# Kernel optimization log

Measured on AMD Instinct MI355X. Metric: run time of the kernel, lower is better.

Reference implementation:

```python
import jax, jax.numpy as jnp
import numpy as np

N_NODES = 349525  # complete 4-ary tree, depth 10: (4**10 - 1) / 3
X_SIZE = 128
H_SIZE = 128


def setup_inputs() -> dict:
    key = jax.random.key(0)
    ks = jax.random.split(key, 6)
    s = 0.05  # keep gates out of saturation
    return {
        "x": jax.random.normal(ks[0], (N_NODES, X_SIZE), jnp.float32),
        "W_iou": jax.random.normal(ks[1], (X_SIZE, 3 * H_SIZE), jnp.float32) * s,
        "U_iou": jax.random.normal(ks[2], (H_SIZE, 3 * H_SIZE), jnp.float32) * s,
        "b_iou": jnp.zeros((3 * H_SIZE,), jnp.float32),
        "W_f": jax.random.normal(ks[3], (X_SIZE, H_SIZE), jnp.float32) * s,
        "U_f": jax.random.normal(ks[4], (H_SIZE, H_SIZE), jnp.float32) * s,
        "b_f": jnp.zeros((H_SIZE,), jnp.float32),
        "depth": 10,
        "branching": 4,
    }


def _apply_node(iou, c_sum):
    # apply_node_func: i,o,u gates then cell/hidden update
    i, o, u = jnp.split(iou, 3, axis=-1)
    c = jax.nn.sigmoid(i) * jnp.tanh(u) + c_sum
    h = jax.nn.sigmoid(o) * jnp.tanh(c)
    return h, c


def reference(x, W_iou, U_iou, b_iou, W_f, U_f, b_f, depth, branching):
    # Nodes are in BFS order of a complete `branching`-ary forest-tree;
    # level l occupies [off[l], off[l+1]) and the children of level l are
    # exactly level l+1 (contiguous, `branching` per parent).
    H = b_f.shape[-1]
    off = [(branching ** l - 1) // (branching - 1) for l in range(depth + 1)]

    node_iou = x @ W_iou + b_iou  # [N, 3H]  (W_iou(x) + b_iou)
    node_f = x @ W_f + b_f        # [N, H]   (W_f(x) + b_f)

    h_levels = [None] * depth
    c_levels = [None] * depth

    # Leaves: mailbox empty -> h_tilda = 0, c = 0
    s, e = off[depth - 1], off[depth]
    h, c = _apply_node(node_iou[s:e], jnp.zeros((e - s, H), x.dtype))
    h_levels[depth - 1], c_levels[depth - 1] = h, c

    # Bottom-up topological propagation
    for l in range(depth - 2, -1, -1):
        s, e = off[l], off[l + 1]
        nl = e - s
        ch_h = h_levels[l + 1].reshape(nl, branching, H)  # mailbox['h']
        ch_c = c_levels[l + 1].reshape(nl, branching, H)  # mailbox['c']
        h_tilda = ch_h.sum(axis=1)
        # f = sigmoid(U_f(mailbox.h) + node_f[:, None])
        f = jax.nn.sigmoid(jnp.einsum("nkh,hg->nkg", ch_h, U_f) + node_f[s:e][:, None, :])
        c_sum = (f * ch_c).sum(axis=1)
        iou = node_iou[s:e] + h_tilda @ U_iou
        h, c = _apply_node(iou, c_sum)
        h_levels[l], c_levels[l] = h, c

    h_all = jnp.concatenate(h_levels, axis=0)
    c_all = jnp.concatenate(c_levels, axis=0)
    return h_all, c_all
```

## Files before the change

kernel.cpp:

```cpp
#include <hip/hip_runtime.h>

#define H 128

typedef __bf16 bf16x8 __attribute__((ext_vector_type(8)));
typedef float f32x4 __attribute__((ext_vector_type(4)));

__device__ __forceinline__ float fsig(float x) {
  return __builtin_amdgcn_rcpf(1.0f + __expf(-x));
}
__device__ __forceinline__ float ftanh(float x) {
  float ax = fabsf(x), e = __expf(-2.0f * ax);
  float t = (1.0f - e) * __builtin_amdgcn_rcpf(1.0f + e);
  return x < 0.0f ? -t : t;
}
__device__ __forceinline__ uint2 pack4(float a, float b, float c, float d) {
  union { __bf16 h[4]; uint2 u; } r;
  r.h[0] = (__bf16)a; r.h[1] = (__bf16)b; r.h[2] = (__bf16)c; r.h[3] = (__bf16)d;
  return r.u;
}
__device__ __forceinline__ unsigned swz(unsigned row, unsigned colByte, unsigned rowBytes) {
  return (row * rowBytes + colByte) ^ ((row & 7) << 4);
}
__device__ __forceinline__ void gload_lds16(const void* g, void* lds) {
  __builtin_amdgcn_global_load_lds((const __attribute__((address_space(1))) void*)g,
                                   (__attribute__((address_space(3))) void*)lds, 16, 0, 0);
}

__global__ __launch_bounds__(256)
void prep_weights(const float* __restrict__ W_iou, const float* __restrict__ U_iou,
                  const float* __restrict__ W_f, const float* __restrict__ U_f,
                  uint4* __restrict__ ws)
{
  int item = blockIdx.x * 256 + threadIdx.x;
  float v[8];
  if (item < 2048) {
    int fj = item >> 8, rem = item & 255, ks = rem >> 6, lane = rem & 63;
    int n = fj * 16 + (lane & 15), kb = ks * 32 + (lane >> 4) * 8;
    #pragma unroll
    for (int j = 0; j < 8; j++) v[j] = U_f[(kb + j) * H + n];
  } else if (item < 4096) {
    int i2 = item - 2048;
    int fj = i2 >> 8, rem = i2 & 255, ks = rem >> 6, lane = rem & 63;
    int n = fj * 16 + (lane & 15), kb = ks * 32 + (lane >> 4) * 8;
    #pragma unroll
    for (int j = 0; j < 8; j++) v[j] = W_f[(kb + j) * H + n];
  } else {
    int i2 = item - 4096;
    int fj = i2 >> 9, rem = i2 & 511, ks = rem >> 6, lane = rem & 63;
    int col = (fj >> 3) * 128 + (fj & 7) * 16 + (lane & 15);
    int kb = ks * 32 + (lane >> 4) * 8;
    #pragma unroll
    for (int j = 0; j < 8; j++) {
      int k = kb + j;
      v[j] = (k < 128) ? W_iou[k * 384 + col] : U_iou[(k - 128) * 384 + col];
    }
  }
  union { __bf16 h[8]; uint4 u; } r;
  #pragma unroll
  for (int j = 0; j < 8; j++) r.h[j] = (__bf16)v[j];
  ws[item] = r.u;
}

__device__ __forceinline__ bf16x8 read_a_f32(const char* As, int row, int colB) {
  unsigned x1 = (unsigned)row * 512 + ((unsigned)colB ^ ((row & 7) << 4));
  unsigned x2 = (unsigned)row * 512 + ((unsigned)(colB + 16) ^ ((row & 7) << 4));
  f32x4 va = *reinterpret_cast<const f32x4*>(As + x1);
  f32x4 vb = *reinterpret_cast<const f32x4*>(As + x2);
  union { __bf16 h[8]; bf16x8 v; } u;
  u.h[0] = (__bf16)va.x; u.h[1] = (__bf16)va.y; u.h[2] = (__bf16)va.z; u.h[3] = (__bf16)va.w;
  u.h[4] = (__bf16)vb.x; u.h[5] = (__bf16)vb.y; u.h[6] = (__bf16)vb.z; u.h[7] = (__bf16)vb.w;
  return u.v;
}

template<bool WS>
__global__ __launch_bounds__(256)
void leaf6(const float* __restrict__ x, const __bf16* __restrict__ iou_fmt,
           const float* __restrict__ b_iou,
           float* __restrict__ h_glob, float* __restrict__ c_glob,
           __bf16* __restrict__ hbf, __bf16* __restrict__ htws, int leaf_start)
{
  __shared__ __align__(16) char As[64 * 512];
  const int t = threadIdx.x;
  const int bid = blockIdx.x;
  const int m0 = leaf_start + bid * 64;
  const int lane = t & 63, w = t >> 6;
  const int l15 = lane & 15, l4 = lane >> 4;

  {
    const char* xb = (const char*)(x + (size_t)m0 * H);
    #pragma unroll
    for (int i = 0; i < 8; i++) {
      int d = w * 8192 + i * 1024 + lane * 16;
      int row = d >> 9, c = d & 511;
      gload_lds16(xb + row * 512 + (c ^ ((row & 7) << 4)), As + w * 8192 + i * 1024);
    }
  }
  __syncthreads();

  #pragma unroll 1
  for (int j = 0; j < 2; j++) {
    f32x4 acc[4][3] = {};
    #pragma unroll
    for (int ks = 0; ks < 4; ks++) {
      bf16x8 a[4], b[3];
      #pragma unroll
      for (int m = 0; m < 4; m++)
        a[m] = read_a_f32(As, m * 16 + l15, ks * 128 + l4 * 32);
      #pragma unroll
      for (int g = 0; g < 3; g++) {
        int nf = g * 8 + 2 * w + j;
        b[g] = *reinterpret_cast<const bf16x8*>(iou_fmt + ((size_t)(nf * 8 + ks) * 64 + lane) * 8);
      }
      #pragma unroll
      for (int m = 0; m < 4; m++)
        #pragma unroll
        for (int g = 0; g < 3; g++)
          acc[m][g] = __builtin_amdgcn_mfma_f32_16x16x32_bf16(a[m], b[g], acc[m][g], 0, 0, 0);
    }

    int ch = (2 * w + j) * 16 + l15;
    float bi = b_iou[ch], bo = b_iou[H + ch], bu = b_iou[2 * H + ch];
    #pragma unroll
    for (int m = 0; m < 4; m++) {
      int rowb = m * 16 + l4 * 4;
      float hsum = 0.0f;
      #pragma unroll
      for (int r = 0; r < 4; r++) {
        size_t o = (size_t)(m0 + rowb + r) * H + ch;
        float c = fsig(acc[m][0][r] + bi) * ftanh(acc[m][2][r] + bu);
        float h = fsig(acc[m][1][r] + bo) * ftanh(c);
        h_glob[o] = h;
        c_glob[o] = c;
        if (WS) {
          int CR = bid * 64 + rowb + r;
          unsigned off = ((unsigned)(CR >> 7)) * 32768u + swz(CR & 127, ch * 2, 256);
          *reinterpret_cast<__bf16*>(reinterpret_cast<char*>(hbf) + off) = (__bf16)h;
          hsum += h;
        }
      }
      if (WS) htws[(size_t)(bid * 16 + m * 4 + l4) * H + ch] = (__bf16)hsum;
    }
  }
}

__device__ __forceinline__ void fused_core(
    const __bf16* __restrict__ uf_fmt, const __bf16* __restrict__ wf_fmt,
    const __bf16* __restrict__ iou_fmt,
    const float* __restrict__ b_iou, const float* __restrict__ b_f,
    float* __restrict__ h_glob, float* __restrict__ c_glob,
    int prow0, int crow0, int npar,
    char* CH, char* XH, float* SC)
{
  const int t = threadIdx.x;
  const int lane = t & 63, w = t >> 6;
  const int l15 = lane & 15, l4 = lane >> 4;

  {
    f32x4 acc[2][2] = {};
    #pragma unroll
    for (int ks = 0; ks < 4; ks++) {
      bf16x8 a[2], b[2];
      #pragma unroll
      for (int m = 0; m < 2; m++)
        a[m] = *reinterpret_cast<const bf16x8*>(XH + swz(m * 16 + l15, (ks * 32 + l4 * 8) * 2, 512));
      #pragma unroll
      for (int n = 0; n < 2; n++) {
        int nf = 2 * w + n;
        b[n] = *reinterpret_cast<const bf16x8*>(wf_fmt + ((size_t)(nf * 4 + ks) * 64 + lane) * 8);
      }
      #pragma unroll
      for (int m = 0; m < 2; m++)
        #pragma unroll
        for (int n = 0; n < 2; n++)
          acc[m][n] = __builtin_amdgcn_mfma_f32_16x16x32_bf16(a[m], b[n], acc[m][n], 0, 0, 0);
    }
    #pragma unroll
    for (int m = 0; m < 2; m++)
      #pragma unroll
      for (int n = 0; n < 2; n++)
        #pragma unroll
        for (int r = 0; r < 4; r++)
          SC[(m * 16 + l4 * 4 + r) * 128 + (2 * w + n) * 16 + l15] = acc[m][n][r];
  }
  __syncthreads();

  {
    f32x4 acc[2][8] = {};
    #pragma unroll
    for (int ks = 0; ks < 4; ks++) {
      bf16x8 a[2], b[8];
      #pragma unroll
      for (int m = 0; m < 2; m++)
        a[m] = *reinterpret_cast<const bf16x8*>(CH + swz(w * 32 + m * 16 + l15, (ks * 32 + l4 * 8) * 2, 256));
      #pragma unroll
      for (int n = 0; n < 8; n++)
        b[n] = *reinterpret_cast<const bf16x8*>(uf_fmt + ((size_t)(n * 4 + ks) * 64 + lane) * 8);
      #pragma unroll
      for (int m = 0; m < 2; m++)
        #pragma unroll
        for (int n = 0; n < 8; n++)
          acc[m][n] = __builtin_amdgcn_mfma_f32_16x16x32_bf16(a[m], b[n], acc[m][n], 0, 0, 0);
    }
    #pragma unroll
    for (int m = 0; m < 2; m++) {
      int rbase = w * 32 + m * 16 + l4 * 4;
      int ploc = rbase >> 2;
      #pragma unroll
      for (int n = 0; n < 8; n++) {
        int ch = n * 16 + l15;
        float sfx = SC[ploc * 128 + ch] + b_f[ch];
        float cs = 0.0f;
        #pragma unroll
        for (int r = 0; r < 4; r++) {
          float f = fsig(acc[m][n][r] + sfx);
          cs = fmaf(f, c_glob[(size_t)(crow0 + rbase + r) * H + ch], cs);
        }
        SC[ploc * 128 + ch] = cs;
      }
    }
  }
  __syncthreads();

  {
    f32x4 acc[2][3][2] = {};
    #pragma unroll
    for (int ks = 0; ks < 8; ks++) {
      bf16x8 a[2], b[3][2];
      #pragma unroll
      for (int m = 0; m < 2; m++)
        a[m] = *reinterpret_cast<const bf16x8*>(XH + swz(m * 16 + l15, (ks * 32 + l4 * 8) * 2, 512));
      #pragma unroll
      for (int g = 0; g < 3; g++)
        #pragma unroll
        for (int j = 0; j < 2; j++) {
          int nf = g * 8 + 2 * w + j;
          b[g][j] = *reinterpret_cast<const bf16x8*>(iou_fmt + ((size_t)(nf * 8 + ks) * 64 + lane) * 8);
        }
      #pragma unroll
      for (int m = 0; m < 2; m++)
        #pragma unroll
        for (int g = 0; g < 3; g++)
          #pragma unroll
          for (int j = 0; j < 2; j++)
            acc[m][g][j] = __builtin_amdgcn_mfma_f32_16x16x32_bf16(a[m], b[g][j], acc[m][g][j], 0, 0, 0);
    }
    #pragma unroll
    for (int j = 0; j < 2; j++) {
      int ch = (2 * w + j) * 16 + l15;
      float bi = b_iou[ch], bo = b_iou[H + ch], bu = b_iou[2 * H + ch];
      #pragma unroll
      for (int m = 0; m < 2; m++) {
        #pragma unroll
        for (int r = 0; r < 4; r++) {
          int ploc = m * 16 + l4 * 4 + r;
          if (ploc < npar) {
            float gi = acc[m][0][j][r] + bi;
            float go = acc[m][1][j][r] + bo;
            float gu = acc[m][2][j][r] + bu;
            float cs = SC[ploc * 128 + ch];
            float c = fsig(gi) * ftanh(gu) + cs;
            float h = fsig(go) * ftanh(c);
            size_t o = (size_t)(prow0 + ploc) * H + ch;
            h_glob[o] = h;
            c_glob[o] = c;
          }
        }
      }
    }
  }
}

__device__ __forceinline__ void fused_body(
    const float* __restrict__ x, const __bf16* __restrict__ uf_fmt,
    const __bf16* __restrict__ wf_fmt, const __bf16* __restrict__ iou_fmt,
    const float* __restrict__ b_iou, const float* __restrict__ b_f,
    float* __restrict__ h_glob, float* __restrict__ c_glob,
    int prow0, int crow0, int npar,
    char* CH, char* XH, float* SC)
{
  const int t = threadIdx.x;
  #pragma unroll
  for (int i = 0; i < 4; i++) {
    int idx = t + i * 256;
    int p = idx >> 5, k0 = (idx & 31) << 2;
    f32x4 s = {};
    #pragma unroll
    for (int j = 0; j < 4; j++) {
      f32x4 v = *reinterpret_cast<const f32x4*>(&h_glob[(size_t)(crow0 + p * 4 + j) * H + k0]);
      *reinterpret_cast<uint2*>(CH + swz(p * 4 + j, k0 * 2, 256)) = pack4(v.x, v.y, v.z, v.w);
      s += v;
    }
    *reinterpret_cast<uint2*>(XH + swz(p, (128 + k0) * 2, 512)) = pack4(s.x, s.y, s.z, s.w);
  }
  #pragma unroll
  for (int i = 0; i < 4; i++) {
    int idx = t + i * 256;
    int p = idx >> 5, k0 = (idx & 31) << 2;
    f32x4 v = *reinterpret_cast<const f32x4*>(&x[(size_t)(prow0 + p) * H + k0]);
    *reinterpret_cast<uint2*>(XH + swz(p, k0 * 2, 512)) = pack4(v.x, v.y, v.z, v.w);
  }
  __syncthreads();
  fused_core(uf_fmt, wf_fmt, iou_fmt, b_iou, b_f, h_glob, c_glob,
             prow0, crow0, npar, CH, XH, SC);
}

__global__ __launch_bounds__(256)
void fused_level_ws(const float* __restrict__ x, const __bf16* __restrict__ uf_fmt,
                    const __bf16* __restrict__ wf_fmt, const __bf16* __restrict__ iou_fmt,
                    const float* __restrict__ b_iou, const float* __restrict__ b_f,
                    float* __restrict__ h_glob, float* __restrict__ c_glob,
                    const __bf16* __restrict__ hbf, const __bf16* __restrict__ htws,
                    int pstart, int cstart)
{
  __shared__ __align__(16) char CH[128 * 256];
  __shared__ __align__(16) char XH[32 * 512];
  __shared__ float SC[32 * 128];
  const int t = threadIdx.x;
  const int bid = blockIdx.x;
  const int lane = t & 63, w = t >> 6;

  {
    const char* src = reinterpret_cast<const char*>(hbf) + (size_t)bid * 32768;
    #pragma unroll
    for (int i = 0; i < 8; i++) {
      int o = w * 8192 + i * 1024;
      gload_lds16(src + o + lane * 16, CH + o);
    }
  }
  #pragma unroll
  for (int i = 0; i < 4; i++) {
    int idx = t + i * 256;
    int p = idx >> 5, k0 = (idx & 31) << 2;
    f32x4 v = *reinterpret_cast<const f32x4*>(&x[(size_t)(pstart + bid * 32 + p) * H + k0]);
    *reinterpret_cast<uint2*>(XH + swz(p, k0 * 2, 512)) = pack4(v.x, v.y, v.z, v.w);
  }
  #pragma unroll
  for (int i = 0; i < 2; i++) {
    int q = t * 2 + i;
    int p = q >> 4, cb = (q & 15) * 16;
    uint4 v = *reinterpret_cast<const uint4*>(
        reinterpret_cast<const char*>(htws) + (size_t)(bid * 32 + p) * 256 + cb);
    *reinterpret_cast<uint4*>(XH + p * 512 + ((256 + cb) ^ ((p & 7) << 4))) = v;
  }
  __syncthreads();

  fused_core(uf_fmt, wf_fmt, iou_fmt, b_iou, b_f, h_glob, c_glob,
             pstart + bid * 32, cstart + bid * 128, 32, CH, XH, SC);
}

__global__ __launch_bounds__(256)
void fused_level(const float* __restrict__ x, const __bf16* __restrict__ uf_fmt,
                 const __bf16* __restrict__ wf_fmt, const __bf16* __restrict__ iou_fmt,
                 const float* __restrict__ b_iou, const float* __restrict__ b_f,
                 float* __restrict__ h_glob, float* __restrict__ c_glob,
                 int pstart, int cstart)
{
  __shared__ __align__(16) char CH[128 * 256];
  __shared__ __align__(16) char XH[32 * 512];
  __shared__ float SC[32 * 128];
  fused_body(x, uf_fmt, wf_fmt, iou_fmt, b_iou, b_f, h_glob, c_glob,
             pstart + blockIdx.x * 32, cstart + blockIdx.x * 128, 32, CH, XH, SC);
}

#define SNR 4
#define SRP 2
#define BR 4

__global__ __launch_bounds__(256)
void small_kernel(const float* __restrict__ x,
                  const float* __restrict__ W_iou, const float* __restrict__ b_iou,
                  const float* __restrict__ U_iou, const float* __restrict__ W_f,
                  const float* __restrict__ U_f, const float* __restrict__ b_f,
                  float* __restrict__ h_out, float* __restrict__ c_out,
                  int lvl_start, int child_start, int n_lvl)
{
  __shared__ float xs[SNR][H];
  __shared__ float hs[SNR * BR][H];
  __shared__ float ht[SNR][H];
  const int t = threadIdx.x;
  const int node0 = blockIdx.x * SNR;
  const int nrows = min(SNR, n_lvl - node0);

  {
    const f32x4* xgv = reinterpret_cast<const f32x4*>(x + (size_t)(lvl_start + node0) * H);
    f32x4* xsv = reinterpret_cast<f32x4*>(&xs[0][0]);
    int total = nrows * (H / 4);
    for (int i = t; i < total; i += 256) xsv[i] = xgv[i];
  }
  {
    const f32x4* hgv = reinterpret_cast<const f32x4*>(h_out + (size_t)(child_start + node0 * BR) * H);
    f32x4* hsv = reinterpret_cast<f32x4*>(&hs[0][0]);
    int total = nrows * BR * (H / 4);
    for (int i = t; i < total; i += 256) hsv[i] = hgv[i];
  }
  __syncthreads();

  const int ch = t & (H - 1);
  const int g = t >> 7;

  float fx[SRP], ai[SRP], ao[SRP], au[SRP];
  {
    float bi = b_iou[ch], bo = b_iou[ch + H], bu = b_iou[ch + 2 * H], bf = b_f[ch];
    #pragma unroll
    for (int r = 0; r < SRP; r++) { fx[r] = bf; ai[r] = bi; ao[r] = bo; au[r] = bu; }
  }
  {
    const float* wfp = W_f + ch;
    const float* wip = W_iou + ch;
    #pragma unroll 4
    for (int k = 0; k < H; k++) {
      float wf = wfp[k * H];
      float w0 = wip[k * 384], w1 = wip[k * 384 + H], w2 = wip[k * 384 + 2 * H];
      #pragma unroll
      for (int r = 0; r < SRP; r++) {
        float xk = xs[g * SRP + r][k];
        fx[r] = fmaf(xk, wf, fx[r]);
        ai[r] = fmaf(xk, w0, ai[r]);
        ao[r] = fmaf(xk, w1, ao[r]);
        au[r] = fmaf(xk, w2, au[r]);
      }
    }
  }
  #pragma unroll
  for (int r = 0; r < SRP; r++) {
    int row = g * SRP + r;
    float s = hs[row * BR + 0][ch] + hs[row * BR + 1][ch]
            + hs[row * BR + 2][ch] + hs[row * BR + 3][ch];
    ht[row][ch] = s;
  }
  __syncthreads();

  float z[BR][SRP];
  #pragma unroll
  for (int kc = 0; kc < BR; kc++)
    #pragma unroll
    for (int r = 0; r < SRP; r++) z[kc][r] = fx[r];
  {
    const float* ufp = U_f + ch;
    #pragma unroll 4
    for (int m = 0; m < H; m++) {
      float uf = ufp[m * H];
      #pragma unroll
      for (int kc = 0; kc < BR; kc++)
        #pragma unroll
        for (int r = 0; r < SRP; r++)
          z[kc][r] = fmaf(hs[(g * SRP + r) * BR + kc][m], uf, z[kc][r]);
    }
  }
  float csum[SRP];
  #pragma unroll
  for (int r = 0; r < SRP; r++) csum[r] = 0.0f;
  #pragma unroll
  for (int kc = 0; kc < BR; kc++) {
    #pragma unroll
    for (int r = 0; r < SRP; r++) {
      size_t childnode = (size_t)child_start + (size_t)(node0 + g * SRP + r) * BR + kc;
      float f = fsig(z[kc][r]);
      csum[r] = fmaf(f, c_out[childnode * H + ch], csum[r]);
    }
  }
  {
    const float* uip = U_iou + ch;
    #pragma unroll 4
    for (int m = 0; m < H; m++) {
      float w0 = uip[m * 384], w1 = uip[m * 384 + H], w2 = uip[m * 384 + 2 * H];
      #pragma unroll
      for (int r = 0; r < SRP; r++) {
        float hm = ht[g * SRP + r][m];
        ai[r] = fmaf(hm, w0, ai[r]);
        ao[r] = fmaf(hm, w1, ao[r]);
        au[r] = fmaf(hm, w2, au[r]);
      }
    }
  }
  #pragma unroll
  for (int r = 0; r < SRP; r++) {
    int row = g * SRP + r;
    if (row < nrows) {
      float c = fsig(ai[r]) * ftanh(au[r]) + csum[r];
      float h = fsig(ao[r]) * ftanh(c);
      size_t node = (size_t)(lvl_start + node0 + row);
      h_out[node * H + ch] = h;
      c_out[node * H + ch] = c;
    }
  }
}

extern "C" void kernel_launch(void* const* d_in, const int* in_sizes, int n_in,
                              void* d_out, int out_size, void* d_ws, size_t ws_size,
                              hipStream_t stream)
{
  const float* x     = (const float*)d_in[0];
  const float* W_iou = (const float*)d_in[1];
  const float* U_iou = (const float*)d_in[2];
  const float* b_iou = (const float*)d_in[3];
  const float* W_f   = (const float*)d_in[4];
  const float* U_f   = (const float*)d_in[5];
  const float* b_f   = (const float*)d_in[6];
  const int N = 349525;

  float* h_out = (float*)d_out;
  float* c_out = h_out + (size_t)N * H;

  const __bf16* uf_fmt  = (const __bf16*)d_ws;
  const __bf16* wf_fmt  = (const __bf16*)d_ws + 16384;
  const __bf16* iou_fmt = (const __bf16*)d_ws + 32768;
  __bf16* hbf  = (__bf16*)((char*)d_ws + 262144);
  __bf16* htws = (__bf16*)((char*)d_ws + 262144 + 67108864);

  const bool use_ws = ws_size >= (262144ULL + 67108864ULL + 16777216ULL);

  int off[11];
  off[0] = 0;
  for (int l = 1; l <= 10; l++) off[l] = off[l - 1] * 4 + 1;

  prep_weights<<<64, 256, 0, stream>>>(W_iou, U_iou, W_f, U_f, (uint4*)d_ws);

  if (use_ws) {
    leaf6<true><<<4096, 256, 0, stream>>>(x, iou_fmt, b_iou, h_out, c_out, hbf, htws, off[9]);
    fused_level_ws<<<2048, 256, 0, stream>>>(x, uf_fmt, wf_fmt, iou_fmt, b_iou, b_f,
                                             h_out, c_out, hbf, htws, off[8], off[9]);
  } else {
    leaf6<false><<<4096, 256, 0, stream>>>(x, iou_fmt, b_iou, h_out, c_out, nullptr, nullptr, off[9]);
    fused_level<<<2048, 256, 0, stream>>>(x, uf_fmt, wf_fmt, iou_fmt, b_iou, b_f,
                                          h_out, c_out, off[8], off[9]);
  }

  for (int l = 7; l >= 4; l--) {
    int n_par = off[l + 1] - off[l];
    fused_level<<<n_par / 32, 256, 0, stream>>>(x, uf_fmt, wf_fmt, iou_fmt, b_iou, b_f,
                                                h_out, c_out, off[l], off[l + 1]);
  }

  for (int l = 3; l >= 0; l--) {
    int s = off[l], e = off[l + 1];
    int n = e - s;
    int grid = (n + SNR - 1) / SNR;
    small_kernel<<<grid, 256, 0, stream>>>(x, W_iou, b_iou, U_iou, W_f, U_f, b_f,
                                           h_out, c_out, s, e, n);
  }
}
```

Baseline: 402.3 us.

## Stage leaf x as bf16 in LDS and pass bf16 child h to two levels

The leaf kernel now loads x with ordinary loads and converts it to bf16 in LDS, replacing the fp32 global_load_lds path and per-MFMA conversion. It then writes a contiguous bf16 copy of h through LDS with coalesced 16-byte stores, and no longer keeps a separate precomputed child-sum buffer. A new fused_hb kernel reads that bf16 h, computes the child sums in LDS, and at level 8 also emits bf16 h for level 7. Levels 8 and 7 therefore avoid re-reading fp32 h from global memory. The cost is extra LDS passes and syncs, plus an in-kernel sum of bf16 values that was previously done in fp32 before rounding.

```diff
diff --git a/kernel.cpp b/kernel.cpp
--- a/kernel.cpp
+++ b/kernel.cpp
@@ -18,12 +18,11 @@
   r.h[0] = (__bf16)a; r.h[1] = (__bf16)b; r.h[2] = (__bf16)c; r.h[3] = (__bf16)d;
   return r.u;
 }
+__device__ __forceinline__ unsigned short bfbits(float h) {
+  union { __bf16 b; unsigned short u; } cv; cv.b = (__bf16)h; return cv.u;
+}
 __device__ __forceinline__ unsigned swz(unsigned row, unsigned colByte, unsigned rowBytes) {
   return (row * rowBytes + colByte) ^ ((row & 7) << 4);
-}
-__device__ __forceinline__ void gload_lds16(const void* g, void* lds) {
-  __builtin_amdgcn_global_load_lds((const __attribute__((address_space(1))) void*)g,
-                                   (__attribute__((address_space(3))) void*)lds, 16, 0, 0);
 }
 
 __global__ __launch_bounds__(256)
@@ -61,69 +60,63 @@
   ws[item] = r.u;
 }
 
-__device__ __forceinline__ bf16x8 read_a_f32(const char* As, int row, int colB) {
-  unsigned x1 = (unsigned)row * 512 + ((unsigned)colB ^ ((row & 7) << 4));
-  unsigned x2 = (unsigned)row * 512 + ((unsigned)(colB + 16) ^ ((row & 7) << 4));
-  f32x4 va = *reinterpret_cast<const f32x4*>(As + x1);
-  f32x4 vb = *reinterpret_cast<const f32x4*>(As + x2);
-  union { __bf16 h[8]; bf16x8 v; } u;
-  u.h[0] = (__bf16)va.x; u.h[1] = (__bf16)va.y; u.h[2] = (__bf16)va.z; u.h[3] = (__bf16)va.w;
-  u.h[4] = (__bf16)vb.x; u.h[5] = (__bf16)vb.y; u.h[6] = (__bf16)vb.z; u.h[7] = (__bf16)vb.w;
-  return u.v;
+__device__ __forceinline__ void leaf_half(const char* As, const __bf16* __restrict__ iou_fmt,
+                                          int j, int w, int l15, int l4, int lane,
+                                          f32x4 (&acc)[4][3])
+{
+  #pragma unroll
+  for (int ks = 0; ks < 4; ks++) {
+    bf16x8 a[4], b[3];
+    #pragma unroll
+    for (int m = 0; m < 4; m++)
+      a[m] = *reinterpret_cast<const bf16x8*>(As + swz(m * 16 + l15, (ks * 32 + l4 * 8) * 2, 256));
+    #pragma unroll
+    for (int g = 0; g < 3; g++) {
+      int nf = g * 8 + 2 * w + j;
+      b[g] = *reinterpret_cast<const bf16x8*>(iou_fmt + ((size_t)(nf * 8 + ks) * 64 + lane) * 8);
+    }
+    #pragma unroll
+    for (int m = 0; m < 4; m++)
+      #pragma unroll
+      for (int g = 0; g < 3; g++)
+        acc[m][g] = __builtin_amdgcn_mfma_f32_16x16x32_bf16(a[m], b[g], acc[m][g], 0, 0, 0);
+  }
 }
 
 template<bool WS>
 __global__ __launch_bounds__(256)
-void leaf6(const float* __restrict__ x, const __bf16* __restrict__ iou_fmt,
+void leaf8(const float* __restrict__ x, const __bf16* __restrict__ iou_fmt,
            const float* __restrict__ b_iou,
            float* __restrict__ h_glob, float* __restrict__ c_glob,
-           __bf16* __restrict__ hbf, __bf16* __restrict__ htws, int leaf_start)
-{
-  __shared__ __align__(16) char As[64 * 512];
+           __bf16* __restrict__ hb_dst, int leaf_start)
+{
+  __shared__ __align__(16) char As[64 * 256];
   const int t = threadIdx.x;
   const int bid = blockIdx.x;
   const int m0 = leaf_start + bid * 64;
   const int lane = t & 63, w = t >> 6;
   const int l15 = lane & 15, l4 = lane >> 4;
 
-  {
-    const char* xb = (const char*)(x + (size_t)m0 * H);
-    #pragma unroll
-    for (int i = 0; i < 8; i++) {
-      int d = w * 8192 + i * 1024 + lane * 16;
-      int row = d >> 9, c = d & 511;
-      gload_lds16(xb + row * 512 + (c ^ ((row & 7) << 4)), As + w * 8192 + i * 1024);
-    }
-  }
-  __syncthreads();
-
-  #pragma unroll 1
-  for (int j = 0; j < 2; j++) {
+  #pragma unroll
+  for (int i = 0; i < 8; i++) {
+    int idx = t + i * 256;
+    int r = idx >> 5, k0 = (idx & 31) << 2;
+    f32x4 v = *reinterpret_cast<const f32x4*>(&x[(size_t)(m0 + r) * H + k0]);
+    *reinterpret_cast<uint2*>(As + swz(r, k0 * 2, 256)) = pack4(v.x, v.y, v.z, v.w);
+  }
+  __syncthreads();
+
+  unsigned hj0p[8];
+
+  {
     f32x4 acc[4][3] = {};
-    #pragma unroll
-    for (int ks = 0; ks < 4; ks++) {
-      bf16x8 a[4], b[3];
-      #pragma unroll
-      for (int m = 0; m < 4; m++)
-        a[m] = read_a_f32(As, m * 16 + l15, ks * 128 + l4 * 32);
-      #pragma unroll
-      for (int g = 0; g < 3; g++) {
-        int nf = g * 8 + 2 * w + j;
-        b[g] = *reinterpret_cast<const bf16x8*>(iou_fmt + ((size_t)(nf * 8 + ks) * 64 + lane) * 8);
-      }
-      #pragma unroll
-      for (int m = 0; m < 4; m++)
-        #pragma unroll
-        for (int g = 0; g < 3; g++)
-          acc[m][g] = __builtin_amdgcn_mfma_f32_16x16x32_bf16(a[m], b[g], acc[m][g], 0, 0, 0);
-    }
-
-    int ch = (2 * w + j) * 16 + l15;
+    leaf_half(As, iou_fmt, 0, w, l15, l4, lane, acc);
+    int ch = 2 * w * 16 + l15;
     float bi = b_iou[ch], bo = b_iou[H + ch], bu = b_iou[2 * H + ch];
     #pragma unroll
     for (int m = 0; m < 4; m++) {
       int rowb = m * 16 + l4 * 4;
-      float hsum = 0.0f;
+      unsigned hv[4];
       #pragma unroll
       for (int r = 0; r < 4; r++) {
         size_t o = (size_t)(m0 + rowb + r) * H + ch;
@@ -131,18 +124,61 @@
         float h = fsig(acc[m][1][r] + bo) * ftanh(c);
         h_glob[o] = h;
         c_glob[o] = c;
-        if (WS) {
-          int CR = bid * 64 + rowb + r;
-          unsigned off = ((unsigned)(CR >> 7)) * 32768u + swz(CR & 127, ch * 2, 256);
-          *reinterpret_cast<__bf16*>(reinterpret_cast<char*>(hbf) + off) = (__bf16)h;
-          hsum += h;
-        }
-      }
-      if (WS) htws[(size_t)(bid * 16 + m * 4 + l4) * H + ch] = (__bf16)hsum;
-    }
-  }
-}
-
+        if (WS) hv[r] = bfbits(h);
+      }
+      if (WS) {
+        hj0p[m * 2 + 0] = hv[0] | (hv[1] << 16);
+        hj0p[m * 2 + 1] = hv[2] | (hv[3] << 16);
+      }
+    }
+  }
+
+  {
+    f32x4 acc[4][3] = {};
+    leaf_half(As, iou_fmt, 1, w, l15, l4, lane, acc);
+    __syncthreads();
+    int ch = (2 * w + 1) * 16 + l15;
+    float bi = b_iou[ch], bo = b_iou[H + ch], bu = b_iou[2 * H + ch];
+    #pragma unroll
+    for (int m = 0; m < 4; m++) {
+      int rowb = m * 16 + l4 * 4;
+      #pragma unroll
+      for (int r = 0; r < 4; r++) {
+        size_t o = (size_t)(m0 + rowb + r) * H + ch;
+        float c = fsig(acc[m][0][r] + bi) * ftanh(acc[m][2][r] + bu);
+        float h = fsig(acc[m][1][r] + bo) * ftanh(c);
+        h_glob[o] = h;
+        c_glob[o] = c;
+        if (WS)
+          *reinterpret_cast<unsigned short*>(As + swz(rowb + r, ch * 2, 256)) = bfbits(h);
+      }
+    }
+  }
+
+  if (WS) {
+    int ch0 = 2 * w * 16 + l15;
+    #pragma unroll
+    for (int m = 0; m < 4; m++) {
+      int rowb = m * 16 + l4 * 4;
+      #pragma unroll
+      for (int r = 0; r < 4; r++) {
+        unsigned hv = hj0p[m * 2 + (r >> 1)] >> ((r & 1) * 16);
+        *reinterpret_cast<unsigned short*>(As + swz(rowb + r, ch0 * 2, 256)) = (unsigned short)hv;
+      }
+    }
+    __syncthreads();
+    char* dst = reinterpret_cast<char*>(hb_dst) + (size_t)bid * 64 * 256;
+    #pragma unroll
+    for (int i = 0; i < 4; i++) {
+      int idx = t + i * 256;
+      int row = idx >> 4, chunk = idx & 15;
+      uint4 v = *reinterpret_cast<const uint4*>(As + swz(row, chunk * 16, 256));
+      *reinterpret_cast<uint4*>(dst + row * 256 + chunk * 16) = v;
+    }
+  }
+}
+
+template<bool HB>
 __device__ __forceinline__ void fused_core(
     const __bf16* __restrict__ uf_fmt, const __bf16* __restrict__ wf_fmt,
     const __bf16* __restrict__ iou_fmt,
@@ -263,9 +299,79 @@
             size_t o = (size_t)(prow0 + ploc) * H + ch;
             h_glob[o] = h;
             c_glob[o] = c;
+            if (HB)
+              *reinterpret_cast<unsigned short*>(CH + swz(ploc, ch * 2, 256)) = bfbits(h);
           }
         }
       }
+    }
+  }
+}
+
+template<bool WRITE_HB>
+__global__ __launch_bounds__(256)
+void fused_hb(const float* __restrict__ x, const __bf16* __restrict__ uf_fmt,
+              const __bf16* __restrict__ wf_fmt, const __bf16* __restrict__ iou_fmt,
+              const float* __restrict__ b_iou, const float* __restrict__ b_f,
+              float* __restrict__ h_glob, float* __restrict__ c_glob,
+              const __bf16* __restrict__ ch_src, __bf16* __restrict__ hb_dst,
+              int pstart, int cstart)
+{
+  __shared__ __align__(16) char CH[128 * 256];
+  __shared__ __align__(16) char XH[32 * 512];
+  __shared__ float SC[32 * 128];
+  const int t = threadIdx.x;
+  const int bid = blockIdx.x;
+
+  {
+    const char* csrc = reinterpret_cast<const char*>(ch_src) + (size_t)bid * 128 * 256;
+    #pragma unroll
+    for (int i = 0; i < 8; i++) {
+      int idx = t + i * 256;
+      int row = idx >> 4, chunk = idx & 15;
+      uint4 v = *reinterpret_cast<const uint4*>(csrc + row * 256 + chunk * 16);
+      *reinterpret_cast<uint4*>(CH + swz(row, chunk * 16, 256)) = v;
+    }
+  }
+  #pragma unroll
+  for (int i = 0; i < 4; i++) {
+    int idx = t + i * 256;
+    int p = idx >> 5, k0 = (idx & 31) << 2;
+    f32x4 v = *reinterpret_cast<const f32x4*>(&x[(size_t)(pstart + bid * 32 + p) * H + k0]);
+    *reinterpret_cast<uint2*>(XH + swz(p, k0 * 2, 512)) = pack4(v.x, v.y, v.z, v.w);
+  }
+  __syncthreads();
+  #pragma unroll
+  for (int i = 0; i < 2; i++) {
+    int idx = t + i * 256;
+    int p = idx >> 4, chunk = idx & 15;
+    float s[8] = {};
+    #pragma unroll
+    for (int cj = 0; cj < 4; cj++) {
+      union { uint4 u; __bf16 h[8]; } uv;
+      uv.u = *reinterpret_cast<const uint4*>(CH + swz(4 * p + cj, chunk * 16, 256));
+      #pragma unroll
+      for (int e = 0; e < 8; e++) s[e] += (float)uv.h[e];
+    }
+    union { __bf16 h[8]; uint4 u; } ov;
+    #pragma unroll
+    for (int e = 0; e < 8; e++) ov.h[e] = (__bf16)s[e];
+    *reinterpret_cast<uint4*>(XH + swz(p, 256 + chunk * 16, 512)) = ov.u;
+  }
+  __syncthreads();
+
+  fused_core<WRITE_HB>(uf_fmt, wf_fmt, iou_fmt, b_iou, b_f, h_glob, c_glob,
+                       pstart + bid * 32, cstart + bid * 128, 32, CH, XH, SC);
+
+  if (WRITE_HB) {
+    __syncthreads();
+    char* dst = reinterpret_cast<char*>(hb_dst) + (size_t)bid * 32 * 256;
+    #pragma unroll
+    for (int i = 0; i < 2; i++) {
+      int idx = t + i * 256;
+      int row = idx >> 4, chunk = idx & 15;
+      uint4 v = *reinterpret_cast<const uint4*>(CH + swz(row, chunk * 16, 256));
+      *reinterpret_cast<uint4*>(dst + row * 256 + chunk * 16) = v;
     }
   }
 }
@@ -300,52 +406,8 @@
     *reinterpret_cast<uint2*>(XH + swz(p, k0 * 2, 512)) = pack4(v.x, v.y, v.z, v.w);
   }
   __syncthreads();
-  fused_core(uf_fmt, wf_fmt, iou_fmt, b_iou, b_f, h_glob, c_glob,
-             prow0, crow0, npar, CH, XH, SC);
-}
-
-__global__ __launch_bounds__(256)
-void fused_level_ws(const float* __restrict__ x, const __bf16* __restrict__ uf_fmt,
-                    const __bf16* __restrict__ wf_fmt, const __bf16* __restrict__ iou_fmt,
-                    const float* __restrict__ b_iou, const float* __restrict__ b_f,
-                    float* __restrict__ h_glob, float* __restrict__ c_glob,
-                    const __bf16* __restrict__ hbf, const __bf16* __restrict__ htws,
-                    int pstart, int cstart)
-{
-  __shared__ __align__(16) char CH[128 * 256];
-  __shared__ __align__(16) char XH[32 * 512];
-  __shared__ float SC[32 * 128];
-  const int t = threadIdx.x;
-  const int bid = blockIdx.x;
-  const int lane = t & 63, w = t >> 6;
-
-  {
-    const char* src = reinterpret_cast<const char*>(hbf) + (size_t)bid * 32768;
-    #pragma unroll
-    for (int i = 0; i < 8; i++) {
-      int o = w * 8192 + i * 1024;
-      gload_lds16(src + o + lane * 16, CH + o);
-    }
-  }
-  #pragma unroll
-  for (int i = 0; i < 4; i++) {
-    int idx = t + i * 256;
-    int p = idx >> 5, k0 = (idx & 31) << 2;
-    f32x4 v = *reinterpret_cast<const f32x4*>(&x[(size_t)(pstart + bid * 32 + p) * H + k0]);
-    *reinterpret_cast<uint2*>(XH + swz(p, k0 * 2, 512)) = pack4(v.x, v.y, v.z, v.w);
-  }
-  #pragma unroll
-  for (int i = 0; i < 2; i++) {
-    int q = t * 2 + i;
-    int p = q >> 4, cb = (q & 15) * 16;
-    uint4 v = *reinterpret_cast<const uint4*>(
-        reinterpret_cast<const char*>(htws) + (size_t)(bid * 32 + p) * 256 + cb);
-    *reinterpret_cast<uint4*>(XH + p * 512 + ((256 + cb) ^ ((p & 7) << 4))) = v;
-  }
-  __syncthreads();
-
-  fused_core(uf_fmt, wf_fmt, iou_fmt, b_iou, b_f, h_glob, c_glob,
-             pstart + bid * 32, cstart + bid * 128, 32, CH, XH, SC);
+  fused_core<false>(uf_fmt, wf_fmt, iou_fmt, b_iou, b_f, h_glob, c_glob,
+                    prow0, crow0, npar, CH, XH, SC);
 }
 
 __global__ __launch_bounds__(256)
@@ -505,10 +567,10 @@
   const __bf16* uf_fmt  = (const __bf16*)d_ws;
   const __bf16* wf_fmt  = (const __bf16*)d_ws + 16384;
   const __bf16* iou_fmt = (const __bf16*)d_ws + 32768;
-  __bf16* hbf  = (__bf16*)((char*)d_ws + 262144);
-  __bf16* htws = (__bf16*)((char*)d_ws + 262144 + 67108864);
-
-  const bool use_ws = ws_size >= (262144ULL + 67108864ULL + 16777216ULL);
+  __bf16* hb16 = (__bf16*)((char*)d_ws + 262144);
+  __bf16* hb_l8 = hb16 + (size_t)262144 * 128;
+
+  const bool use_ws = ws_size >= (262144ULL + 83886080ULL);
 
   int off[11];
   off[0] = 0;
@@ -517,16 +579,20 @@
   prep_weights<<<64, 256, 0, stream>>>(W_iou, U_iou, W_f, U_f, (uint4*)d_ws);
 
   if (use_ws) {
-    leaf6<true><<<4096, 256, 0, stream>>>(x, iou_fmt, b_iou, h_out, c_out, hbf, htws, off[9]);
-    fused_level_ws<<<2048, 256, 0, stream>>>(x, uf_fmt, wf_fmt, iou_fmt, b_iou, b_f,
-                                             h_out, c_out, hbf, htws, off[8], off[9]);
+    leaf8<true><<<4096, 256, 0, stream>>>(x, iou_fmt, b_iou, h_out, c_out, hb16, off[9]);
+    fused_hb<true><<<2048, 256, 0, stream>>>(x, uf_fmt, wf_fmt, iou_fmt, b_iou, b_f,
+                                             h_out, c_out, hb16, hb_l8, off[8], off[9]);
+    fused_hb<false><<<512, 256, 0, stream>>>(x, uf_fmt, wf_fmt, iou_fmt, b_iou, b_f,
+                                             h_out, c_out, hb_l8, nullptr, off[7], off[8]);
   } else {
-    leaf6<false><<<4096, 256, 0, stream>>>(x, iou_fmt, b_iou, h_out, c_out, nullptr, nullptr, off[9]);
+    leaf8<false><<<4096, 256, 0, stream>>>(x, iou_fmt, b_iou, h_out, c_out, nullptr, off[9]);
     fused_level<<<2048, 256, 0, stream>>>(x, uf_fmt, wf_fmt, iou_fmt, b_iou, b_f,
                                           h_out, c_out, off[8], off[9]);
-  }
-
-  for (int l = 7; l >= 4; l--) {
+    fused_level<<<512, 256, 0, stream>>>(x, uf_fmt, wf_fmt, iou_fmt, b_iou, b_f,
+                                         h_out, c_out, off[7], off[8]);
+  }
+
+  for (int l = 6; l >= 4; l--) {
     int n_par = off[l + 1] - off[l];
     fused_level<<<n_par / 32, 256, 0, stream>>>(x, uf_fmt, wf_fmt, iou_fmt, b_iou, b_f,
                                                 h_out, c_out, off[l], off[l + 1]);
```

Result: faster. 384.9 us (median of 2 runs) (-4.3%).
